# Performance work log

Measured on AMD Instinct MI355X. Metric: run time of the kernel, lower is better.

Reference implementation:

```python
import jax, jax.numpy as jnp
import numpy as np

D_MODEL = 1024
NUM_HEADS = 16
D_K = D_MODEL // NUM_HEADS
B, S = 2, 2048


def setup_inputs() -> dict:
    key = jax.random.key(0)
    ks = jax.random.split(key, 9)
    sc = 1.0 / np.sqrt(D_MODEL)
    return {
        "x": jax.random.normal(ks[0], (B, S, D_MODEL), dtype=jnp.float32),
        "Wq": jax.random.normal(ks[1], (D_MODEL, D_MODEL), dtype=jnp.float32) * sc,
        "bq": jnp.zeros((D_MODEL,), dtype=jnp.float32),
        "Wk": jax.random.normal(ks[2], (D_MODEL, D_MODEL), dtype=jnp.float32) * sc,
        "bk": jnp.zeros((D_MODEL,), dtype=jnp.float32),
        "Wv": jax.random.normal(ks[3], (D_MODEL, D_MODEL), dtype=jnp.float32) * sc,
        "bv": jnp.zeros((D_MODEL,), dtype=jnp.float32),
        "Wo": jax.random.normal(ks[4], (D_MODEL, D_MODEL), dtype=jnp.float32) * sc,
        "bo": jnpp if False else jnp.zeros((D_MODEL,), dtype=jnp.float32),
    }


def reference(x, Wq, bq, Wk, bk, Wv, bv, Wo, bo):
    b, s, d = x.shape
    # projections, split heads: (B, H, S, Dk)
    def heads(t):
        return t.reshape(b, s, NUM_HEADS, D_K).transpose(0, 2, 1, 3)
    Q = heads(x @ Wq + bq)
    K = heads(x @ Wk + bk)
    V = heads(x @ Wv + bv)
    scores = jnp.einsum("bhqd,bhkd->bhqk", Q, K) / jnp.sqrt(jnp.float32(D_K))
    attn = jax.nn.softmax(scores, axis=-1)
    out = jnp.einsum("bhqk,bhkd->bhqd", attn, V)
    out = out.transpose(0, 2, 1, 3).reshape(b, s, d)
    return out @ Wo + bo
```

## Files before the change

kernel.cpp:

```cpp
#include <hip/hip_runtime.h>
#include <hip/hip_bf16.h>


#define SEQ 2048
#define DMODEL 1024
#define NHEAD 16
#define DK 64
#define NBATCH 2
#define NBH 32
#define MTOT 4096

typedef __attribute__((ext_vector_type(4))) float  f32x4;
typedef __attribute__((ext_vector_type(8))) short  bf16x8;
typedef __attribute__((ext_vector_type(4))) short  bf16x4;
typedef __attribute__((ext_vector_type(4))) unsigned short u16x4;

#define QSCALE 0.18033688f

__device__ __forceinline__ unsigned short f2bf(float x) {
  union { __hip_bfloat16 h; unsigned short u; } cv;
  cv.h = __float2bfloat16(x);
  return cv.u;
}

#define EXP2(x) __builtin_amdgcn_exp2f(x)

__device__ __forceinline__ void gload16(const void* g, void* l) {
  __builtin_amdgcn_global_load_lds(
      (const __attribute__((address_space(1))) unsigned int*)g,
      (__attribute__((address_space(3))) unsigned int*)l, 16, 0, 0);
}

__device__ __forceinline__ f32x4 vmax4(f32x4 a, f32x4 b) {
  f32x4 r;
  r[0] = fmaxf(a[0], b[0]); r[1] = fmaxf(a[1], b[1]);
  r[2] = fmaxf(a[2], b[2]); r[3] = fmaxf(a[3], b[3]);
  return r;
}

__global__ __launch_bounds__(256) void conv_x(const float* __restrict__ X,
                                              unsigned short* __restrict__ Xb) {
  size_t i = ((size_t)blockIdx.x * 256 + threadIdx.x) * 4;
  f32x4 v = *(const f32x4*)&X[i];
  u16x4 pk;
  pk[0] = f2bf(v[0]); pk[1] = f2bf(v[1]); pk[2] = f2bf(v[2]); pk[3] = f2bf(v[3]);
  *(u16x4*)&Xb[i] = pk;
}

__global__ __launch_bounds__(256) void conv_wt(
    const float* __restrict__ W0, const float* __restrict__ W1,
    const float* __restrict__ W2, const float* __restrict__ W3,
    unsigned short* __restrict__ T0, unsigned short* __restrict__ T1,
    unsigned short* __restrict__ T2, unsigned short* __restrict__ T3) {
  const float* W; unsigned short* T;
  switch (blockIdx.z) {
    case 0: W = W0; T = T0; break;
    case 1: W = W1; T = T1; break;
    case 2: W = W2; T = T2; break;
    default: W = W3; T = T3; break;
  }
  __shared__ float tile[64][65];
  const int k0 = blockIdx.x * 64, n0 = blockIdx.y * 64;
  const int tr = threadIdx.x >> 4, tc = (threadIdx.x & 15) * 4;
#pragma unroll
  for (int i = 0; i < 4; ++i) {
    int r = tr + i * 16;
    f32x4 v = *(const f32x4*)&W[(size_t)(k0 + r) * DMODEL + n0 + tc];
    tile[r][tc + 0] = v[0]; tile[r][tc + 1] = v[1];
    tile[r][tc + 2] = v[2]; tile[r][tc + 3] = v[3];
  }
  __syncthreads();
#pragma unroll
  for (int i = 0; i < 4; ++i) {
    int nr = tr + i * 16;
    u16x4 pk;
    pk[0] = f2bf(tile[tc + 0][nr]); pk[1] = f2bf(tile[tc + 1][nr]);
    pk[2] = f2bf(tile[tc + 2][nr]); pk[3] = f2bf(tile[tc + 3][nr]);
    *(u16x4*)&T[(size_t)(n0 + nr) * DMODEL + k0 + tc] = pk;
  }
}

__global__ __launch_bounds__(256) void gemm_qkv(
    const short* __restrict__ A, const short* __restrict__ Bt,
    const float* __restrict__ bq, const float* __restrict__ bk,
    const float* __restrict__ bv, unsigned short* __restrict__ Qg,
    unsigned short* __restrict__ Kg, unsigned short* __restrict__ Vtg) {
  const int tid = threadIdx.x;
  const int lane = tid & 63, w = tid >> 6;
  const int lq = lane & 15, g = lane >> 4;
  const int m0 = blockIdx.y * 128, n0 = blockIdx.x * 128;
  const int wm = (w >> 1) * 64, wn = (w & 1) * 64;
  const int which = n0 >> 10;

  __shared__ __attribute__((aligned(16))) short abuf[128 * 64];
  __shared__ __attribute__((aligned(16))) short bbuf[128 * 64];

  f32x4 acc[4][4] = {};
  const char* Ab = (const char*)A;
  const char* Bb = (const char*)Bt;

  for (int kt = 0; kt < 16; ++kt) {
    __syncthreads();
#pragma unroll
    for (int i = 0; i < 4; ++i) {
      int y = tid * 16 + i * 4096;
      int row = y >> 7, cb = y & 127;
      gload16(Ab + (size_t)(m0 + row) * 2048 + kt * 128 + cb, (char*)abuf + y);
      gload16(Bb + (size_t)(n0 + row) * 2048 + kt * 128 + cb, (char*)bbuf + y);
    }
    __syncthreads();
#pragma unroll
    for (int ks = 0; ks < 2; ++ks) {
      bf16x8 af[4], bfr[4];
#pragma unroll
      for (int i = 0; i < 4; ++i) {
        af[i]  = *(const bf16x8*)&abuf[(wm + i * 16 + lq) * 64 + ks * 32 + g * 8];
        bfr[i] = *(const bf16x8*)&bbuf[(wn + i * 16 + lq) * 64 + ks * 32 + g * 8];
      }
#pragma unroll
      for (int mi = 0; mi < 4; ++mi)
#pragma unroll
        for (int ni = 0; ni < 4; ++ni)
          acc[mi][ni] = __builtin_amdgcn_mfma_f32_16x16x32_bf16(
              af[mi], bfr[ni], acc[mi][ni], 0, 0, 0);
    }
  }

  const float* bias = (which == 0) ? bq : (which == 1) ? bk : bv;
  unsigned short* o = (which == 0) ? Qg : (which == 1) ? Kg : Vtg;
  const float sc = (which == 0) ? QSCALE : 1.0f;

#pragma unroll
  for (int mi = 0; mi < 4; ++mi) {
#pragma unroll
    for (int ni = 0; ni < 4; ++ni) {
      const int nl = (n0 & 1023) + wn + ni * 16 + lq;
      const int mbase = m0 + wm + mi * 16 + g * 4;
      const float bs = bias[nl];
      const int h = nl >> 6, d = nl & 63;
      if (which == 2) {
        const int b = mbase >> 11, s = mbase & 2047;
        u16x4 pk;
#pragma unroll
        for (int r = 0; r < 4; ++r) pk[r] = f2bf(acc[mi][ni][r] + bs);
        *(u16x4*)&o[(size_t)((b * NHEAD + h) * DK + d) * SEQ + s] = pk;
      } else {
#pragma unroll
        for (int r = 0; r < 4; ++r) {
          const int m = mbase + r;
          const int b = m >> 11, s = m & 2047;
          o[(size_t)((b * NHEAD + h) * SEQ + s) * DK + d] =
              f2bf((acc[mi][ni][r] + bs) * sc);
        }
      }
    }
  }
}

__global__ __launch_bounds__(256) void gemm_out(const short* __restrict__ A,
                                                const short* __restrict__ Bt,
                                                const float* __restrict__ bias,
                                                float* __restrict__ o) {
  const int tid = threadIdx.x;
  const int lane = tid & 63, w = tid >> 6;
  const int lq = lane & 15, g = lane >> 4;
  const int m0 = blockIdx.y * 128, n0 = blockIdx.x * 128;
  const int wm = (w >> 1) * 64, wn = (w & 1) * 64;

  __shared__ __attribute__((aligned(16))) short abuf[128 * 64];
  __shared__ __attribute__((aligned(16))) short bbuf[128 * 64];

  f32x4 acc[4][4] = {};
  const char* Ab = (const char*)A;
  const char* Bb = (const char*)Bt;

  for (int kt = 0; kt < 16; ++kt) {
    __syncthreads();
#pragma unroll
    for (int i = 0; i < 4; ++i) {
      int y = tid * 16 + i * 4096;
      int row = y >> 7, cb = y & 127;
      gload16(Ab + (size_t)(m0 + row) * 2048 + kt * 128 + cb, (char*)abuf + y);
      gload16(Bb + (size_t)(n0 + row) * 2048 + kt * 128 + cb, (char*)bbuf + y);
    }
    __syncthreads();
#pragma unroll
    for (int ks = 0; ks < 2; ++ks) {
      bf16x8 af[4], bfr[4];
#pragma unroll
      for (int i = 0; i < 4; ++i) {
        af[i]  = *(const bf16x8*)&abuf[(wm + i * 16 + lq) * 64 + ks * 32 + g * 8];
        bfr[i] = *(const bf16x8*)&bbuf[(wn + i * 16 + lq) * 64 + ks * 32 + g * 8];
      }
#pragma unroll
      for (int mi = 0; mi < 4; ++mi)
#pragma unroll
        for (int ni = 0; ni < 4; ++ni)
          acc[mi][ni] = __builtin_amdgcn_mfma_f32_16x16x32_bf16(
              af[mi], bfr[ni], acc[mi][ni], 0, 0, 0);
    }
  }

#pragma unroll
  for (int mi = 0; mi < 4; ++mi) {
#pragma unroll
    for (int ni = 0; ni < 4; ++ni) {
      const int n = n0 + wn + ni * 16 + lq;
      const int mbase = m0 + wm + mi * 16 + g * 4;
      const float bs = bias[n];
#pragma unroll
      for (int r = 0; r < 4; ++r)
        o[(size_t)(mbase + r) * DMODEL + n] = acc[mi][ni][r] + bs;
    }
  }
}

__global__ __launch_bounds__(256) void attn_kernel(
    const short* __restrict__ Qg, const short* __restrict__ Kg,
    const short* __restrict__ Vtg, unsigned short* __restrict__ Og) {
  const int tid = threadIdx.x, lane = tid & 63, w = tid >> 6;
  const int lq = lane & 15, g = lane >> 4;
  const int q0 = blockIdx.x * 64, bh = blockIdx.y;

  __shared__ __attribute__((aligned(16))) short kbuf[2][64 * 64];
  __shared__ __attribute__((aligned(16))) short vbuf[2][64 * 64];
  __shared__ __attribute__((aligned(16))) short pbuf[4 * 1024];

  const short* qrow = Qg + ((size_t)bh * SEQ + q0 + w * 16 + lq) * DK;
  bf16x8 qf[2];
  qf[0] = *(const bf16x8*)&qrow[g * 8];
  qf[1] = *(const bf16x8*)&qrow[32 + g * 8];

  f32x4 oacc[4] = {};
  float m_run = -3.0e38f, l_run = 0.f;

  const char* kbase = (const char*)(Kg + (size_t)bh * SEQ * DK);
  const char* vbase = (const char*)(Vtg + (size_t)bh * DK * SEQ);
  const int sw = (lq & 7) << 4;

  const int y0 = tid * 16, y1 = y0 + 4096;
  const int r0 = y0 >> 7, r1 = y1 >> 7;
  const int c0 = (y0 ^ (r0 << 4)) & 0x70;
  const int c1 = (y1 ^ (r1 << 4)) & 0x70;
  const int ksrc0 = (y0 & ~0x70) | c0;
  const int ksrc1 = (y1 & ~0x70) | c1;
  const int vsrc0 = r0 * 4096 + c0;
  const int vsrc1 = r1 * 4096 + c1;

#define STAGE(T, BI)                                                      \
  do {                                                                    \
    gload16(kbase + (size_t)(T) * 8192 + ksrc0, (char*)kbuf[BI] + y0);    \
    gload16(kbase + (size_t)(T) * 8192 + ksrc1, (char*)kbuf[BI] + y1);    \
    gload16(vbase + vsrc0 + (size_t)(T) * 128, (char*)vbuf[BI] + y0);     \
    gload16(vbase + vsrc1 + (size_t)(T) * 128, (char*)vbuf[BI] + y1);     \
  } while (0)

  STAGE(0, 0);

  for (int t = 0; t < 32; ++t) {
    const int bi = t & 1;
    __syncthreads();
    if (t < 31) STAGE(t + 1, bi ^ 1);

    const char* kb = (const char*)kbuf[bi];
    const char* vb = (const char*)vbuf[bi];

    f32x4 sv[4];
    __builtin_amdgcn_s_setprio(1);
#pragma unroll
    for (int kt2 = 0; kt2 < 4; ++kt2) {
      f32x4 s = {};
#pragma unroll
      for (int ks = 0; ks < 2; ++ks) {
        bf16x8 kf = *(const bf16x8*)(kb + (kt2 * 16 + lq) * 128 +
                                     ((ks * 64 + g * 16) ^ sw));
        s = __builtin_amdgcn_mfma_f32_16x16x32_bf16(kf, qf[ks], s, 0, 0, 0);
      }
      sv[kt2] = s;
    }
    __builtin_amdgcn_s_setprio(0);

    f32x4 mx = vmax4(vmax4(sv[0], sv[1]), vmax4(sv[2], sv[3]));
    float vmax = fmaxf(fmaxf(mx[0], mx[1]), fmaxf(mx[2], mx[3]));
    vmax = fmaxf(vmax, __shfl_xor(vmax, 16));
    vmax = fmaxf(vmax, __shfl_xor(vmax, 32));

    if (!__all(vmax <= m_run + 8.0f)) {
      const float m_new = fmaxf(m_run, vmax);
      const float corr = EXP2(m_run - m_new);
#pragma unroll
      for (int dt = 0; dt < 4; ++dt)
#pragma unroll
        for (int r = 0; r < 4; ++r) oacc[dt][r] *= corr;
      l_run *= corr;
      m_run = m_new;
    }

#pragma unroll
    for (int kt2 = 0; kt2 < 4; ++kt2)
#pragma unroll
      for (int r = 0; r < 4; ++r) sv[kt2][r] = EXP2(sv[kt2][r] - m_run);

    f32x4 s4 = (sv[0] + sv[1]) + (sv[2] + sv[3]);
    float psum = (s4[0] + s4[1]) + (s4[2] + s4[3]);
    psum += __shfl_xor(psum, 16);
    psum += __shfl_xor(psum, 32);
    l_run += psum;

    char* pb = (char*)pbuf + w * 2048 + lq * 128;
#pragma unroll
    for (int kt2 = 0; kt2 < 4; ++kt2) {
      bf16x4 pk;
#pragma unroll
      for (int r = 0; r < 4; ++r) pk[r] = (short)f2bf(sv[kt2][r]);
      *(bf16x4*)(pb + ((kt2 * 32 + g * 8) ^ sw)) = pk;
    }
    asm volatile("" ::: "memory");

    __builtin_amdgcn_s_setprio(1);
#pragma unroll
    for (int ks2 = 0; ks2 < 2; ++ks2) {
      bf16x8 pf = *(const bf16x8*)(pb + ((ks2 * 64 + g * 16) ^ sw));
#pragma unroll
      for (int dt = 0; dt < 4; ++dt) {
        bf16x8 vf = *(const bf16x8*)(vb + (dt * 16 + lq) * 128 +
                                     ((ks2 * 64 + g * 16) ^ sw));
        oacc[dt] = __builtin_amdgcn_mfma_f32_16x16x32_bf16(vf, pf, oacc[dt], 0, 0, 0);
      }
    }
    __builtin_amdgcn_s_setprio(0);
  }
#undef STAGE

  const float inv = 1.0f / l_run;
  const int b = bh >> 4, h = bh & 15;
  const size_t rowbase =
      ((size_t)b * SEQ + q0 + w * 16 + lq) * DMODEL + h * DK;
#pragma unroll
  for (int dt = 0; dt < 4; ++dt) {
    u16x4 pk;
#pragma unroll
    for (int r = 0; r < 4; ++r) pk[r] = f2bf(oacc[dt][r] * inv);
    *(u16x4*)&Og[rowbase + dt * 16 + g * 4] = pk;
  }
}

extern "C" void kernel_launch(void* const* d_in, const int* in_sizes, int n_in,
                              void* d_out, int out_size, void* d_ws,
                              size_t ws_size, hipStream_t stream) {
  const float* x  = (const float*)d_in[0];
  const float* Wq = (const float*)d_in[1];
  const float* bq = (const float*)d_in[2];
  const float* Wk = (const float*)d_in[3];
  const float* bk = (const float*)d_in[4];
  const float* Wv = (const float*)d_in[5];
  const float* bv = (const float*)d_in[6];
  const float* Wo = (const float*)d_in[7];
  const float* bo = (const float*)d_in[8];
  float* out = (float*)d_out;

  char* ws = (char*)d_ws;
  unsigned short* Xb    = (unsigned short*)(ws);
  unsigned short* Wtqkv = (unsigned short*)(ws + (8u << 20));
  unsigned short* Wto   = (unsigned short*)(ws + (14u << 20));
  unsigned short* Qg    = (unsigned short*)(ws + (16u << 20));
  unsigned short* Kg    = (unsigned short*)(ws + (24u << 20));
  unsigned short* Vtg   = (unsigned short*)(ws + (32u << 20));
  unsigned short* Ab    = Xb;

  conv_x<<<dim3(4096), 256, 0, stream>>>(x, Xb);
  conv_wt<<<dim3(16, 16, 4), 256, 0, stream>>>(
      Wq, Wk, Wv, Wo, Wtqkv, Wtqkv + (1u << 20), Wtqkv + (2u << 20), Wto);

  gemm_qkv<<<dim3(24, 32), 256, 0, stream>>>(
      (const short*)Xb, (const short*)Wtqkv, bq, bk, bv, Qg, Kg, Vtg);

  attn_kernel<<<dim3(32, 32), 256, 0, stream>>>(
      (const short*)Qg, (const short*)Kg, (const short*)Vtg, Ab);

  gemm_out<<<dim3(8, 32), 256, 0, stream>>>(
      (const short*)Ab, (const short*)Wto, bo, out);
}
```

Baseline: 156.3 us.

## Load K/V directly from global in attention, fuse conversion kernels, MFMA row sums

The attention kernel drops the LDS double-buffered K/V staging and barriers, loading K and V fragments straight from global memory into registers. Blocks are remapped through a swizzled 1D grid index to improve L2 locality. The softmax row sum is computed with an MFMA against a ones vector instead of shuffles, and the max uses fmax3 chains. The x conversion and weight transpose kernels are merged into one launch. Direct global loads give up LDS sharing of K/V across the four waves, so global and L2 traffic rises and load latency is no longer hidden by prefetching.

```diff
diff --git a/kernel.cpp b/kernel.cpp
--- a/kernel.cpp
+++ b/kernel.cpp
@@ -25,42 +25,45 @@
 
 #define EXP2(x) __builtin_amdgcn_exp2f(x)
 
+__device__ __forceinline__ float fmax3(float a, float b, float c) {
+  return fmaxf(fmaxf(a, b), c);
+}
+
 __device__ __forceinline__ void gload16(const void* g, void* l) {
   __builtin_amdgcn_global_load_lds(
       (const __attribute__((address_space(1))) unsigned int*)g,
       (__attribute__((address_space(3))) unsigned int*)l, 16, 0, 0);
 }
 
-__device__ __forceinline__ f32x4 vmax4(f32x4 a, f32x4 b) {
-  f32x4 r;
-  r[0] = fmaxf(a[0], b[0]); r[1] = fmaxf(a[1], b[1]);
-  r[2] = fmaxf(a[2], b[2]); r[3] = fmaxf(a[3], b[3]);
-  return r;
-}
-
-__global__ __launch_bounds__(256) void conv_x(const float* __restrict__ X,
-                                              unsigned short* __restrict__ Xb) {
-  size_t i = ((size_t)blockIdx.x * 256 + threadIdx.x) * 4;
-  f32x4 v = *(const f32x4*)&X[i];
-  u16x4 pk;
-  pk[0] = f2bf(v[0]); pk[1] = f2bf(v[1]); pk[2] = f2bf(v[2]); pk[3] = f2bf(v[3]);
-  *(u16x4*)&Xb[i] = pk;
-}
-
-__global__ __launch_bounds__(256) void conv_wt(
+__global__ __launch_bounds__(256) void conv_all(
+    const float* __restrict__ X, unsigned short* __restrict__ Xb,
     const float* __restrict__ W0, const float* __restrict__ W1,
     const float* __restrict__ W2, const float* __restrict__ W3,
     unsigned short* __restrict__ T0, unsigned short* __restrict__ T1,
     unsigned short* __restrict__ T2, unsigned short* __restrict__ T3) {
+  __shared__ float tile[64][65];
+  const int b = blockIdx.x;
+  if (b >= 1024) {
+    size_t i = ((size_t)(b - 1024) * 256 + threadIdx.x) * 16;
+#pragma unroll
+    for (int c = 0; c < 4; ++c) {
+      f32x4 v = *(const f32x4*)&X[i + c * 4];
+      u16x4 pk;
+      pk[0] = f2bf(v[0]); pk[1] = f2bf(v[1]);
+      pk[2] = f2bf(v[2]); pk[3] = f2bf(v[3]);
+      *(u16x4*)&Xb[i + c * 4] = pk;
+    }
+    return;
+  }
+  const int z = b >> 8, rem = b & 255;
   const float* W; unsigned short* T;
-  switch (blockIdx.z) {
+  switch (z) {
     case 0: W = W0; T = T0; break;
     case 1: W = W1; T = T1; break;
     case 2: W = W2; T = T2; break;
     default: W = W3; T = T3; break;
   }
-  __shared__ float tile[64][65];
-  const int k0 = blockIdx.x * 64, n0 = blockIdx.y * 64;
+  const int k0 = (rem & 15) * 64, n0 = (rem >> 4) * 64;
   const int tr = threadIdx.x >> 4, tc = (threadIdx.x & 15) * 4;
 #pragma unroll
   for (int i = 0; i < 4; ++i) {
@@ -220,10 +223,10 @@
     const short* __restrict__ Vtg, unsigned short* __restrict__ Og) {
   const int tid = threadIdx.x, lane = tid & 63, w = tid >> 6;
   const int lq = lane & 15, g = lane >> 4;
-  const int q0 = blockIdx.x * 64, bh = blockIdx.y;
-
-  __shared__ __attribute__((aligned(16))) short kbuf[2][64 * 64];
-  __shared__ __attribute__((aligned(16))) short vbuf[2][64 * 64];
+  const int bid = blockIdx.x;
+  const int swz = (bid & 7) * 128 + (bid >> 3);
+  const int bh = swz >> 5, q0 = (swz & 31) * 64;
+
   __shared__ __attribute__((aligned(16))) short pbuf[4 * 1024];
 
   const short* qrow = Qg + ((size_t)bh * SEQ + q0 + w * 16 + lq) * DK;
@@ -231,57 +234,46 @@
   qf[0] = *(const bf16x8*)&qrow[g * 8];
   qf[1] = *(const bf16x8*)&qrow[32 + g * 8];
 
+  bf16x8 ones;
+#pragma unroll
+  for (int j = 0; j < 8; ++j) ones[j] = (short)0x3F80;
+
   f32x4 oacc[4] = {};
   float m_run = -3.0e38f, l_run = 0.f;
 
-  const char* kbase = (const char*)(Kg + (size_t)bh * SEQ * DK);
-  const char* vbase = (const char*)(Vtg + (size_t)bh * DK * SEQ);
+  const short* kp = Kg + (size_t)bh * SEQ * DK + lq * DK + g * 8;
+  const short* vp = Vtg + (size_t)bh * DK * SEQ + lq * SEQ + g * 8;
   const int sw = (lq & 7) << 4;
-
-  const int y0 = tid * 16, y1 = y0 + 4096;
-  const int r0 = y0 >> 7, r1 = y1 >> 7;
-  const int c0 = (y0 ^ (r0 << 4)) & 0x70;
-  const int c1 = (y1 ^ (r1 << 4)) & 0x70;
-  const int ksrc0 = (y0 & ~0x70) | c0;
-  const int ksrc1 = (y1 & ~0x70) | c1;
-  const int vsrc0 = r0 * 4096 + c0;
-  const int vsrc1 = r1 * 4096 + c1;
-
-#define STAGE(T, BI)                                                      \
-  do {                                                                    \
-    gload16(kbase + (size_t)(T) * 8192 + ksrc0, (char*)kbuf[BI] + y0);    \
-    gload16(kbase + (size_t)(T) * 8192 + ksrc1, (char*)kbuf[BI] + y1);    \
-    gload16(vbase + vsrc0 + (size_t)(T) * 128, (char*)vbuf[BI] + y0);     \
-    gload16(vbase + vsrc1 + (size_t)(T) * 128, (char*)vbuf[BI] + y1);     \
-  } while (0)
-
-  STAGE(0, 0);
+  char* pb = (char*)pbuf + w * 2048 + lq * 128;
 
   for (int t = 0; t < 32; ++t) {
-    const int bi = t & 1;
-    __syncthreads();
-    if (t < 31) STAGE(t + 1, bi ^ 1);
-
-    const char* kb = (const char*)kbuf[bi];
-    const char* vb = (const char*)vbuf[bi];
+    const short* kt_p = kp + t * 64 * DK;
+    const short* vt_p = vp + t * 64;
+
+    bf16x8 kf[4][2];
+#pragma unroll
+    for (int kt2 = 0; kt2 < 4; ++kt2)
+#pragma unroll
+      for (int ks = 0; ks < 2; ++ks)
+        kf[kt2][ks] = *(const bf16x8*)&kt_p[kt2 * 16 * DK + ks * 32];
 
     f32x4 sv[4];
     __builtin_amdgcn_s_setprio(1);
 #pragma unroll
     for (int kt2 = 0; kt2 < 4; ++kt2) {
       f32x4 s = {};
-#pragma unroll
-      for (int ks = 0; ks < 2; ++ks) {
-        bf16x8 kf = *(const bf16x8*)(kb + (kt2 * 16 + lq) * 128 +
-                                     ((ks * 64 + g * 16) ^ sw));
-        s = __builtin_amdgcn_mfma_f32_16x16x32_bf16(kf, qf[ks], s, 0, 0, 0);
-      }
+      s = __builtin_amdgcn_mfma_f32_16x16x32_bf16(kf[kt2][0], qf[0], s, 0, 0, 0);
+      s = __builtin_amdgcn_mfma_f32_16x16x32_bf16(kf[kt2][1], qf[1], s, 0, 0, 0);
       sv[kt2] = s;
     }
     __builtin_amdgcn_s_setprio(0);
 
-    f32x4 mx = vmax4(vmax4(sv[0], sv[1]), vmax4(sv[2], sv[3]));
-    float vmax = fmaxf(fmaxf(mx[0], mx[1]), fmaxf(mx[2], mx[3]));
+    float m0a = fmax3(sv[0][0], sv[0][1], sv[0][2]);
+    float m1a = fmax3(sv[0][3], sv[1][0], sv[1][1]);
+    float m2a = fmax3(sv[1][2], sv[1][3], sv[2][0]);
+    float m3a = fmax3(sv[2][1], sv[2][2], sv[2][3]);
+    float m4a = fmax3(sv[3][0], sv[3][1], sv[3][2]);
+    float vmax = fmaxf(fmax3(m0a, m1a, m2a), fmax3(m3a, m4a, sv[3][3]));
     vmax = fmaxf(vmax, __shfl_xor(vmax, 16));
     vmax = fmaxf(vmax, __shfl_xor(vmax, 32));
 
@@ -301,13 +293,6 @@
 #pragma unroll
       for (int r = 0; r < 4; ++r) sv[kt2][r] = EXP2(sv[kt2][r] - m_run);
 
-    f32x4 s4 = (sv[0] + sv[1]) + (sv[2] + sv[3]);
-    float psum = (s4[0] + s4[1]) + (s4[2] + s4[3]);
-    psum += __shfl_xor(psum, 16);
-    psum += __shfl_xor(psum, 32);
-    l_run += psum;
-
-    char* pb = (char*)pbuf + w * 2048 + lq * 128;
 #pragma unroll
     for (int kt2 = 0; kt2 < 4; ++kt2) {
       bf16x4 pk;
@@ -317,20 +302,21 @@
     }
     asm volatile("" ::: "memory");
 
+    f32x4 lsum = {};
     __builtin_amdgcn_s_setprio(1);
 #pragma unroll
     for (int ks2 = 0; ks2 < 2; ++ks2) {
       bf16x8 pf = *(const bf16x8*)(pb + ((ks2 * 64 + g * 16) ^ sw));
+      lsum = __builtin_amdgcn_mfma_f32_16x16x32_bf16(ones, pf, lsum, 0, 0, 0);
 #pragma unroll
       for (int dt = 0; dt < 4; ++dt) {
-        bf16x8 vf = *(const bf16x8*)(vb + (dt * 16 + lq) * 128 +
-                                     ((ks2 * 64 + g * 16) ^ sw));
+        bf16x8 vf = *(const bf16x8*)&vt_p[dt * 16 * SEQ + ks2 * 32];
         oacc[dt] = __builtin_amdgcn_mfma_f32_16x16x32_bf16(vf, pf, oacc[dt], 0, 0, 0);
       }
     }
     __builtin_amdgcn_s_setprio(0);
-  }
-#undef STAGE
+    l_run += lsum[0];
+  }
 
   const float inv = 1.0f / l_run;
   const int b = bh >> 4, h = bh & 15;
@@ -368,14 +354,14 @@
   unsigned short* Vtg   = (unsigned short*)(ws + (32u << 20));
   unsigned short* Ab    = Xb;
 
-  conv_x<<<dim3(4096), 256, 0, stream>>>(x, Xb);
-  conv_wt<<<dim3(16, 16, 4), 256, 0, stream>>>(
-      Wq, Wk, Wv, Wo, Wtqkv, Wtqkv + (1u << 20), Wtqkv + (2u << 20), Wto);
+  conv_all<<<dim3(2048), 256, 0, stream>>>(
+      x, Xb, Wq, Wk, Wv, Wo,
+      Wtqkv, Wtqkv + (1u << 20), Wtqkv + (2u << 20), Wto);
 
   gemm_qkv<<<dim3(24, 32), 256, 0, stream>>>(
       (const short*)Xb, (const short*)Wtqkv, bq, bk, bv, Qg, Kg, Vtg);
 
-  attn_kernel<<<dim3(32, 32), 256, 0, stream>>>(
+  attn_kernel<<<dim3(1024), 256, 0, stream>>>(
       (const short*)Qg, (const short*)Kg, (const short*)Vtg, Ab);
 
   gemm_out<<<dim3(8, 32), 256, 0, stream>>>(
```

Measured after the change: 319.1 us. +104.2%, slower.
